# Kernel tuning notes

Measured on AMD Instinct MI355X. Metric: run time of the kernel, lower is better.

Reference implementation:

```python
import jax, jax.numpy as jnp
import numpy as np

B, S, IN, H, D, OUT = 4, 4096, 1024, 16, 64, 1024


def setup_inputs() -> dict:
    key = jax.random.key(0)
    k1, k2, k3, k4, k5 = jax.random.split(key, 5)
    x = jax.random.normal(k1, (B, S, IN), dtype=jnp.float32)
    input_state = jnp.zeros((B, H, D), dtype=jnp.float32)
    # parameters
    w_in = jax.random.normal(k2, (H * D, IN), dtype=jnp.float32) * (1.0 / np.sqrt(IN))
    state_weight = jax.random.normal(k3, (H, D, D), dtype=jnp.float32) * (1.0 / np.sqrt(D))
    state_bias = jax.random.normal(k4, (H, D), dtype=jnp.float32) * 0.02
    w_out = jax.random.normal(k5, (OUT, H * D), dtype=jnp.float32) * (1.0 / np.sqrt(H * D))
    return {"x": x, "input_state": input_state, "w_in": w_in,
            "state_weight": state_weight, "state_bias": state_bias, "w_out": w_out}


def reference(x, input_state, w_in, state_weight, state_bias, w_out):
    # input projection: [B, S, IN] -> [B, S, H, D]
    xp = jnp.einsum('bsi,ki->bsk', x, w_in).reshape(B, S, H, D)
    xs = jnp.transpose(xp, (1, 0, 2, 3))  # [S, B, H, D] for scan over time

    def step(h, x_t):
        # h: [B, H, D]; per-head recurrence h_t = tanh(W_h h_{t-1} + b + x_t)
        h_new = jnp.tanh(jnp.einsum('hed,bhd->bhe', state_weight, h)
                         + state_bias[None] + x_t)
        return h_new, h_new

    _, ys = jax.lax.scan(step, input_state, xs)  # ys: [S, B, H, D]
    y = jnp.transpose(ys, (1, 0, 2, 3)).reshape(B, S, H * D)
    return jnp.einsum('bsk,ok->bso', y, w_out)
```

## Files before the change

### kernel.cpp

```cpp
#include <hip/hip_runtime.h>

#define B_ 4
#define S_ 4096
#define IN_ 1024
#define H_ 16
#define D_ 64
#define OUT_ 1024
#define HD_ 1024
#define M_ 16384

typedef __bf16 bf16x8 __attribute__((ext_vector_type(8)));
typedef __bf16 bf16x2 __attribute__((ext_vector_type(2)));
typedef float floatx4 __attribute__((ext_vector_type(4)));
typedef int int32x4 __attribute__((ext_vector_type(4)));

#define TWO_LOG2E 2.885390081777927f

static __device__ __forceinline__ unsigned int f2bf(float f) {
    unsigned int u = __builtin_bit_cast(unsigned int, f);
    u += 0x7fffu + ((u >> 16) & 1u);
    return u >> 16;
}

__global__ void cast_f32_bf16(const float* __restrict__ src,
                              unsigned short* __restrict__ dst, int n4) {
    int i = blockIdx.x * blockDim.x + threadIdx.x;
    if (i < n4) {
        float4 v = ((const float4*)src)[i];
        ushort4 o;
        o.x = (unsigned short)f2bf(v.x); o.y = (unsigned short)f2bf(v.y);
        o.z = (unsigned short)f2bf(v.z); o.w = (unsigned short)f2bf(v.w);
        ((ushort4*)dst)[i] = o;
    }
}

__global__ __launch_bounds__(256) void gemm_bt(
    const unsigned short* __restrict__ A,
    const unsigned short* __restrict__ Bm,
    float* __restrict__ C, int M, int N, int K) {
    __shared__ unsigned short As[128 * 32];
    __shared__ unsigned short Bs[128 * 32];
    const int t = threadIdx.x;
    const int lane = t & 63;
    const int wave = t >> 6;
    const int wm = wave >> 1, wn = wave & 1;
    const int m0 = blockIdx.y * 128;
    const int n0 = blockIdx.x * 128;
    const int l16 = lane & 15;
    const int quad = lane >> 4;
    const int r16 = lane >> 2;
    const int kc = lane & 3;

    floatx4 acc[4][4];
#pragma unroll
    for (int i = 0; i < 4; i++)
#pragma unroll
        for (int j = 0; j < 4; j++) acc[i][j] = (floatx4){0.f, 0.f, 0.f, 0.f};

    for (int k0 = 0; k0 < K; k0 += 32) {
#pragma unroll
        for (int it = 0; it < 2; it++) {
            int chunk = wave * 2 + it;
            int row = chunk * 16 + r16;
            const unsigned short* ga = A + (size_t)(m0 + row) * K + k0 + kc * 8;
            __builtin_amdgcn_global_load_lds(
                (const __attribute__((address_space(1))) void*)ga,
                (__attribute__((address_space(3))) void*)(As + chunk * 512),
                16, 0, 0);
            const unsigned short* gb = Bm + (size_t)(n0 + row) * K + k0 + kc * 8;
            __builtin_amdgcn_global_load_lds(
                (const __attribute__((address_space(1))) void*)gb,
                (__attribute__((address_space(3))) void*)(Bs + chunk * 512),
                16, 0, 0);
        }
        __syncthreads();
        bf16x8 af[4], bfr[4];
#pragma unroll
        for (int i = 0; i < 4; i++)
            af[i] = *(const bf16x8*)(As + (wm * 64 + i * 16 + l16) * 32 + quad * 8);
#pragma unroll
        for (int j = 0; j < 4; j++)
            bfr[j] = *(const bf16x8*)(Bs + (wn * 64 + j * 16 + l16) * 32 + quad * 8);
#pragma unroll
        for (int i = 0; i < 4; i++)
#pragma unroll
            for (int j = 0; j < 4; j++)
                acc[i][j] = __builtin_amdgcn_mfma_f32_16x16x32_bf16(
                    af[i], bfr[j], acc[i][j], 0, 0, 0);
        __syncthreads();
    }
#pragma unroll
    for (int i = 0; i < 4; i++)
#pragma unroll
        for (int j = 0; j < 4; j++)
#pragma unroll
            for (int r = 0; r < 4; r++) {
                int row = m0 + wm * 64 + i * 16 + quad * 4 + r;
                int col = n0 + wn * 64 + j * 16 + l16;
                C[(size_t)row * N + col] = acc[i][j][r];
            }
}

__global__ __launch_bounds__(64, 1) void rnn_scan(
    const float* __restrict__ xp,
    const float* __restrict__ w_h,
    const float* __restrict__ bias,
    const float* __restrict__ h0,
    unsigned short* __restrict__ y) {
    const int bh = blockIdx.x;
    const int b = bh >> 4;
    const int h = bh & 15;
    const int e = threadIdx.x;
    const int c = e & 15;
    const int q = e >> 4;

    auto loadB = [&](int nt, int koff) -> bf16x8 {
        const float* wr = w_h + ((size_t)(h * 64 + nt * 16 + c)) * 64 + q * 16 + koff;
        float4 v0 = ((const float4*)wr)[0];
        float4 v1 = ((const float4*)wr)[1];
        int32x4 bi;
        bi[0] = (int)(f2bf(v0.x * TWO_LOG2E) | (f2bf(v0.y * TWO_LOG2E) << 16));
        bi[1] = (int)(f2bf(v0.z * TWO_LOG2E) | (f2bf(v0.w * TWO_LOG2E) << 16));
        bi[2] = (int)(f2bf(v1.x * TWO_LOG2E) | (f2bf(v1.y * TWO_LOG2E) << 16));
        bi[3] = (int)(f2bf(v1.z * TWO_LOG2E) | (f2bf(v1.w * TWO_LOG2E) << 16));
        return __builtin_bit_cast(bf16x8, bi);
    };
    const bf16x8 BfA0 = loadB(0, 0), BfB0 = loadB(0, 8);
    const bf16x8 BfA1 = loadB(1, 0), BfB1 = loadB(1, 8);
    const bf16x8 BfA2 = loadB(2, 0), BfB2 = loadB(2, 8);
    const bf16x8 BfA3 = loadB(3, 0), BfB3 = loadB(3, 8);

    const bool q1 = (q & 1) != 0;
    const bool q2 = (q & 2) != 0;

    const float be = bias[h * 64 + e];
    float hn = h0[(b * 16 + h) * 64 + e];

    const float* xb = xp + ((size_t)(b * S_) * 16 + h) * 64 + e;
    unsigned short* yb = y + ((size_t)(b * S_) * 16 + h) * 64 + e;

    float bxA[8], bxB[8];
#pragma unroll
    for (int i2 = 0; i2 < 8; i2++)
        bxA[i2] = (be + xb[(size_t)i2 * 1024]) * TWO_LOG2E;
#pragma unroll
    for (int i2 = 0; i2 < 8; i2++)
        bxB[i2] = (be + xb[(size_t)(8 + i2) * 1024]) * TWO_LOG2E;

    auto step = [&](int t, float bx) {
        float hs = __builtin_bit_cast(float, __builtin_amdgcn_update_dpp(
            0, __builtin_bit_cast(int, hn), 0xF5, 0xF, 0xF, true));
        unsigned int pk;
        asm("v_cvt_pk_bf16_f32 %0, %1, %2" : "=v"(pk) : "v"(hn), "v"(hs));
        int32x4 a0i, a1i;
        a0i[0] = __builtin_amdgcn_update_dpp(0, (int)pk, 0x150 + 0,  0xF, 0xF, true);
        a0i[1] = __builtin_amdgcn_update_dpp(0, (int)pk, 0x150 + 2,  0xF, 0xF, true);
        a0i[2] = __builtin_amdgcn_update_dpp(0, (int)pk, 0x150 + 4,  0xF, 0xF, true);
        a0i[3] = __builtin_amdgcn_update_dpp(0, (int)pk, 0x150 + 6,  0xF, 0xF, true);
        a1i[0] = __builtin_amdgcn_update_dpp(0, (int)pk, 0x150 + 8,  0xF, 0xF, true);
        a1i[1] = __builtin_amdgcn_update_dpp(0, (int)pk, 0x150 + 10, 0xF, 0xF, true);
        a1i[2] = __builtin_amdgcn_update_dpp(0, (int)pk, 0x150 + 12, 0xF, 0xF, true);
        a1i[3] = __builtin_amdgcn_update_dpp(0, (int)pk, 0x150 + 14, 0xF, 0xF, true);
        bf16x8 A0 = __builtin_bit_cast(bf16x8, a0i);
        bf16x8 A1 = __builtin_bit_cast(bf16x8, a1i);
        const floatx4 z4 = (floatx4){0.f, 0.f, 0.f, 0.f};
        const floatx4 cb = (floatx4){bx, 0.f, 0.f, 0.f};
        floatx4 acA0 = __builtin_amdgcn_mfma_f32_16x16x32_bf16(A0, BfA0, cb, 0, 0, 0);
        floatx4 acB0 = __builtin_amdgcn_mfma_f32_16x16x32_bf16(A1, BfB0, z4, 0, 0, 0);
        floatx4 acA1 = __builtin_amdgcn_mfma_f32_16x16x32_bf16(A0, BfA1, cb, 0, 0, 0);
        floatx4 acB1 = __builtin_amdgcn_mfma_f32_16x16x32_bf16(A1, BfB1, z4, 0, 0, 0);
        floatx4 acA2 = __builtin_amdgcn_mfma_f32_16x16x32_bf16(A0, BfA2, cb, 0, 0, 0);
        floatx4 acB2 = __builtin_amdgcn_mfma_f32_16x16x32_bf16(A1, BfB2, z4, 0, 0, 0);
        floatx4 acA3 = __builtin_amdgcn_mfma_f32_16x16x32_bf16(A0, BfA3, cb, 0, 0, 0);
        floatx4 acB3 = __builtin_amdgcn_mfma_f32_16x16x32_bf16(A1, BfB3, z4, 0, 0, 0);
        float yA01 = q1 ? acA1[0] : acA0[0];
        float yA23 = q1 ? acA3[0] : acA2[0];
        float yA   = q2 ? yA23 : yA01;
        float yB01 = q1 ? acB1[0] : acB0[0];
        float yB23 = q1 ? acB3[0] : acB2[0];
        float yB   = q2 ? yB23 : yB01;
        float pre = yA + yB;
        float em = __builtin_amdgcn_exp2f(pre);
        float r  = __builtin_amdgcn_rcpf(em + 1.0f);
        hn = fmaf(-2.0f, r, 1.0f);
        yb[(size_t)t * 1024] = (unsigned short)f2bf(hn);
    };

    for (int t0 = 0; t0 < S_; t0 += 16) {
#pragma unroll
        for (int u = 0; u < 8; u++) step(t0 + u, bxA[u]);
        if (t0 + 16 < S_) {
#pragma unroll
            for (int i2 = 0; i2 < 8; i2++)
                bxA[i2] = (be + xb[(size_t)(t0 + 16 + i2) * 1024]) * TWO_LOG2E;
        }
#pragma unroll
        for (int u = 0; u < 8; u++) step(t0 + 8 + u, bxB[u]);
        if (t0 + 24 < S_) {
#pragma unroll
            for (int i2 = 0; i2 < 8; i2++)
                bxB[i2] = (be + xb[(size_t)(t0 + 24 + i2) * 1024]) * TWO_LOG2E;
        }
    }
}

extern "C" void kernel_launch(void* const* d_in, const int* in_sizes, int n_in,
                              void* d_out, int out_size, void* d_ws, size_t ws_size,
                              hipStream_t stream) {
    const float* x     = (const float*)d_in[0];
    const float* h0    = (const float*)d_in[1];
    const float* w_in  = (const float*)d_in[2];
    const float* w_h   = (const float*)d_in[3];
    const float* bias  = (const float*)d_in[4];
    const float* w_out = (const float*)d_in[5];
    float* out = (float*)d_out;

    char* ws = (char*)d_ws;
    unsigned short* x_bf    = (unsigned short*)(ws);
    unsigned short* win_bf  = (unsigned short*)(ws + (size_t)33554432);
    unsigned short* wout_bf = (unsigned short*)(ws + (size_t)35651584);
    unsigned short* y_bf    = (unsigned short*)(ws + (size_t)37748736);

    {
        int n4 = (M_ * IN_) / 4;
        cast_f32_bf16<<<(n4 + 255) / 256, 256, 0, stream>>>(x, x_bf, n4);
        int w4 = (HD_ * IN_) / 4;
        cast_f32_bf16<<<(w4 + 255) / 256, 256, 0, stream>>>(w_in, win_bf, w4);
        cast_f32_bf16<<<(w4 + 255) / 256, 256, 0, stream>>>(w_out, wout_bf, w4);
    }
    dim3 g1(HD_ / 128, M_ / 128);
    gemm_bt<<<g1, 256, 0, stream>>>(x_bf, win_bf, out, M_, HD_, IN_);
    rnn_scan<<<64, 64, 0, stream>>>(out, w_h, bias, h0, y_bf);
    dim3 g2(OUT_ / 128, M_ / 128);
    gemm_bt<<<g2, 256, 0, stream>>>(y_bf, wout_bf, out, M_, OUT_, HD_);
}
```

Baseline: 959.5 us.

## Fuse projection GEMMs and RNN scan into one persistent kernel with flag pipelining

The three launches (input GEMM, scan, output GEMM) become one persistent kernel. 64 blocks run the per-(batch, head) recurrence, and 192 worker blocks compute GEMM tiles in time-chunk order. Atomic counters in global memory signal which 128-row chunks of the input projection are ready and which chunks of the scan output are finished, so the GEMMs can overlap with the serial scan. This adds spin-wait synchronisation and a dependence on all 256 blocks being resident at once. It also risks the GEMM memory traffic slowing the latency-bound scan.

```diff
diff --git a/kernel.cpp b/kernel.cpp
--- a/kernel.cpp
+++ b/kernel.cpp
@@ -20,6 +20,14 @@
     unsigned int u = __builtin_bit_cast(unsigned int, f);
     u += 0x7fffu + ((u >> 16) & 1u);
     return u >> 16;
+}
+
+__device__ unsigned int g1cnt[128];
+__device__ unsigned int scan_done[128];
+
+__global__ void zero_flags() {
+    int i = threadIdx.x;
+    if (i < 128) { g1cnt[i] = 0; scan_done[i] = 0; }
 }
 
 __global__ void cast_f32_bf16(const float* __restrict__ src,
@@ -34,18 +42,16 @@
     }
 }
 
-__global__ __launch_bounds__(256) void gemm_bt(
+static __device__ __forceinline__ void gemm_tile(
     const unsigned short* __restrict__ A,
     const unsigned short* __restrict__ Bm,
-    float* __restrict__ C, int M, int N, int K) {
-    __shared__ unsigned short As[128 * 32];
-    __shared__ unsigned short Bs[128 * 32];
+    float* __restrict__ C,
+    int m0, int n0,
+    unsigned short* As, unsigned short* Bs) {
     const int t = threadIdx.x;
     const int lane = t & 63;
     const int wave = t >> 6;
     const int wm = wave >> 1, wn = wave & 1;
-    const int m0 = blockIdx.y * 128;
-    const int n0 = blockIdx.x * 128;
     const int l16 = lane & 15;
     const int quad = lane >> 4;
     const int r16 = lane >> 2;
@@ -57,17 +63,17 @@
 #pragma unroll
         for (int j = 0; j < 4; j++) acc[i][j] = (floatx4){0.f, 0.f, 0.f, 0.f};
 
-    for (int k0 = 0; k0 < K; k0 += 32) {
+    for (int k0 = 0; k0 < 1024; k0 += 32) {
 #pragma unroll
         for (int it = 0; it < 2; it++) {
             int chunk = wave * 2 + it;
             int row = chunk * 16 + r16;
-            const unsigned short* ga = A + (size_t)(m0 + row) * K + k0 + kc * 8;
+            const unsigned short* ga = A + (size_t)(m0 + row) * 1024 + k0 + kc * 8;
             __builtin_amdgcn_global_load_lds(
                 (const __attribute__((address_space(1))) void*)ga,
                 (__attribute__((address_space(3))) void*)(As + chunk * 512),
                 16, 0, 0);
-            const unsigned short* gb = Bm + (size_t)(n0 + row) * K + k0 + kc * 8;
+            const unsigned short* gb = Bm + (size_t)(n0 + row) * 1024 + k0 + kc * 8;
             __builtin_amdgcn_global_load_lds(
                 (const __attribute__((address_space(1))) void*)gb,
                 (__attribute__((address_space(3))) void*)(Bs + chunk * 512),
@@ -97,25 +103,61 @@
             for (int r = 0; r < 4; r++) {
                 int row = m0 + wm * 64 + i * 16 + quad * 4 + r;
                 int col = n0 + wn * 64 + j * 16 + l16;
-                C[(size_t)row * N + col] = acc[i][j][r];
-            }
-}
-
-__global__ __launch_bounds__(64, 1) void rnn_scan(
-    const float* __restrict__ xp,
+                C[(size_t)row * 1024 + col] = acc[i][j][r];
+            }
+}
+
+__global__ __launch_bounds__(256, 1) void fused(
+    const unsigned short* __restrict__ x_bf,
+    const unsigned short* __restrict__ win_bf,
+    const unsigned short* __restrict__ wout_bf,
+    unsigned short* __restrict__ y_bf,
+    float* __restrict__ outp,
     const float* __restrict__ w_h,
     const float* __restrict__ bias,
-    const float* __restrict__ h0,
-    unsigned short* __restrict__ y) {
-    const int bh = blockIdx.x;
+    const float* __restrict__ h0) {
+    __shared__ unsigned short As[128 * 32];
+    __shared__ unsigned short Bs[128 * 32];
+    const int blk = blockIdx.x;
+
+    if (blk >= 64) {
+        const int wid = blk - 64;
+        for (int idx = wid; idx < 2048; idx += 192) {
+            int j = (idx < 1024) ? idx : idx - 1024;
+            int c = j >> 5;
+            int b = (j >> 3) & 3;
+            int n = j & 7;
+            int m0 = (b * 32 + c) * 128;
+            int n0 = n * 128;
+            if (idx < 1024) {
+                gemm_tile(x_bf, win_bf, outp, m0, n0, As, Bs);
+                __syncthreads();
+                if (threadIdx.x == 0)
+                    __hip_atomic_fetch_add(&g1cnt[b * 32 + c], 1u,
+                                           __ATOMIC_RELEASE, __HIP_MEMORY_SCOPE_AGENT);
+            } else {
+                if (threadIdx.x == 0) {
+                    while (__hip_atomic_load(&scan_done[b * 32 + c],
+                                             __ATOMIC_ACQUIRE, __HIP_MEMORY_SCOPE_AGENT) < 16u)
+                        __builtin_amdgcn_s_sleep(16);
+                }
+                __syncthreads();
+                gemm_tile(y_bf, wout_bf, outp, m0, n0, As, Bs);
+            }
+        }
+        return;
+    }
+
+    if (threadIdx.x >= 64) return;
+    const int bh = blk;
     const int b = bh >> 4;
     const int h = bh & 15;
     const int e = threadIdx.x;
-    const int c = e & 15;
+    const int c16 = e & 15;
     const int q = e >> 4;
 
     auto loadB = [&](int nt, int koff) -> bf16x8 {
-        const float* wr = w_h + ((size_t)(h * 64 + nt * 16 + c)) * 64 + q * 16 + koff;
+        const float* wr = w_h + ((size_t)(h * 64 + nt * 16 + c16)) * 64 + q * 16 + koff;
         float4 v0 = ((const float4*)wr)[0];
         float4 v1 = ((const float4*)wr)[1];
         int32x4 bi;
@@ -136,8 +178,16 @@
     const float be = bias[h * 64 + e];
     float hn = h0[(b * 16 + h) * 64 + e];
 
-    const float* xb = xp + ((size_t)(b * S_) * 16 + h) * 64 + e;
-    unsigned short* yb = y + ((size_t)(b * S_) * 16 + h) * 64 + e;
+    const float* xb = outp + ((size_t)(b * S_) * 16 + h) * 64 + e;
+    unsigned short* yb = y_bf + ((size_t)(b * S_) * 16 + h) * 64 + e;
+
+    auto waitg1 = [&](int cc) {
+        const unsigned int* p = &g1cnt[b * 32 + cc];
+        while (__hip_atomic_load(p, __ATOMIC_ACQUIRE, __HIP_MEMORY_SCOPE_AGENT) < 8u)
+            __builtin_amdgcn_s_sleep(16);
+    };
+    waitg1(0);
+    waitg1(1);
 
     float bxA[8], bxB[8];
 #pragma unroll
@@ -186,21 +236,28 @@
         yb[(size_t)t * 1024] = (unsigned short)f2bf(hn);
     };
 
-    for (int t0 = 0; t0 < S_; t0 += 16) {
-#pragma unroll
-        for (int u = 0; u < 8; u++) step(t0 + u, bxA[u]);
-        if (t0 + 16 < S_) {
-#pragma unroll
-            for (int i2 = 0; i2 < 8; i2++)
-                bxA[i2] = (be + xb[(size_t)(t0 + 16 + i2) * 1024]) * TWO_LOG2E;
+    for (int cc = 0; cc < 32; cc++) {
+        if (cc >= 1 && cc + 1 < 32) waitg1(cc + 1);
+        for (int k = 0; k < 8; k++) {
+            int t0 = cc * 128 + k * 16;
+#pragma unroll
+            for (int u = 0; u < 8; u++) step(t0 + u, bxA[u]);
+            if (t0 + 16 < S_) {
+#pragma unroll
+                for (int i2 = 0; i2 < 8; i2++)
+                    bxA[i2] = (be + xb[(size_t)(t0 + 16 + i2) * 1024]) * TWO_LOG2E;
+            }
+#pragma unroll
+            for (int u = 0; u < 8; u++) step(t0 + 8 + u, bxB[u]);
+            if (t0 + 24 < S_) {
+#pragma unroll
+                for (int i2 = 0; i2 < 8; i2++)
+                    bxB[i2] = (be + xb[(size_t)(t0 + 24 + i2) * 1024]) * TWO_LOG2E;
+            }
         }
-#pragma unroll
-        for (int u = 0; u < 8; u++) step(t0 + 8 + u, bxB[u]);
-        if (t0 + 24 < S_) {
-#pragma unroll
-            for (int i2 = 0; i2 < 8; i2++)
-                bxB[i2] = (be + xb[(size_t)(t0 + 24 + i2) * 1024]) * TWO_LOG2E;
-        }
+        if (e == 0)
+            __hip_atomic_fetch_add(&scan_done[b * 32 + cc], 1u,
+                                   __ATOMIC_RELEASE, __HIP_MEMORY_SCOPE_AGENT);
     }
 }
 
@@ -228,9 +285,6 @@
         cast_f32_bf16<<<(w4 + 255) / 256, 256, 0, stream>>>(w_in, win_bf, w4);
         cast_f32_bf16<<<(w4 + 255) / 256, 256, 0, stream>>>(w_out, wout_bf, w4);
     }
-    dim3 g1(HD_ / 128, M_ / 128);
-    gemm_bt<<<g1, 256, 0, stream>>>(x_bf, win_bf, out, M_, HD_, IN_);
-    rnn_scan<<<64, 64, 0, stream>>>(out, w_h, bias, h0, y_bf);
-    dim3 g2(OUT_ / 128, M_ / 128);
-    gemm_bt<<<g2, 256, 0, stream>>>(y_bf, wout_bf, out, M_, OUT_, HD_);
-}
+    zero_flags<<<1, 128, 0, stream>>>();
+    fused<<<256, 256, 0, stream>>>(x_bf, win_bf, wout_bf, y_bf, out, w_h, bias, h0);
+}
```

After: 1.284 ms. 1.34x slower.
